# Kernel tuning notes

Hardware: AMD Instinct MI355X
Metric: run time of the kernel (lower is better)

## Reference

```python
import jax, jax.numpy as jnp
import numpy as np

B, D, T, V = 16, 128, 4096, 1024


def setup_inputs() -> dict:
    key = jax.random.key(0)
    k1, k2 = jax.random.split(key)
    latents = jax.random.normal(k1, (B, D, T), dtype=jnp.float32)
    codebook = jax.random.normal(k2, (V, D), dtype=jnp.float32)  # code_embed.weight
    return {"latents": latents, "codebook": codebook}


def reference(latents, codebook):
    # decode(): latents (B, D, T) -> (B, T, D); nearest code under L2 (torch.cdist + argmin)
    x = jnp.transpose(latents, (0, 2, 1))  # (B, T, D)
    x_sq = jnp.sum(x * x, axis=-1, keepdims=True)          # (B, T, 1)
    c_sq = jnp.sum(codebook * codebook, axis=-1)           # (V,)
    cross = jnp.einsum('btd,vd->btv', x, codebook)         # (B, T, V) -- the fusion target
    d2 = x_sq - 2.0 * cross + c_sq                         # (B, T, V)
    codes = jnp.argmin(d2, axis=-1)                        # (B, T) int
    # quantized latents: embed the chosen codes back to (B, D, T)
    quantized = jnp.transpose(codebook[codes], (0, 2, 1))  # (B, D, T)
    return codes.astype(jnp.int32), quantized
```

## Files before the change

kernel.cpp:

```cpp
#include <hip/hip_runtime.h>

#define B_ 16
#define D_ 128
#define T_ 4096
#define V_ 1024

typedef _Float16 half8 __attribute__((ext_vector_type(8)));
typedef float float4v __attribute__((ext_vector_type(4)));


__global__ __launch_bounds__(256) void split_csq_kernel(const float* __restrict__ cb,
                                                        char* __restrict__ Bc,
                                                        float* __restrict__ chsq) {
    const int g = blockIdx.x * 256 + threadIdx.x;
    const int v = g >> 4;
    const int k0 = (g & 15) << 3;
    const float* src = cb + (size_t)v * D_ + k0;
    half8 h, l;
    float s = 0.f;
#pragma unroll
    for (int j = 0; j < 8; ++j) {
        float c = src[j];
        _Float16 ch = (_Float16)c;
        h[j] = ch;
        l[j] = (_Float16)((c - (float)ch) * 2048.0f);
        s = fmaf(c, c, s);
    }
    const int kt = k0 >> 5;
    const int q = (k0 >> 3) & 3;
    const int c = v >> 5;
    const int ntl = (v >> 4) & 1;
    const int ln = v & 15;
    const size_t off =
        (size_t)c * 16384 + kt * 2048 + ntl * 1024 + (size_t)(q * 16 + ln) * 16;
    *(half8*)(Bc + off) = h;
    *(half8*)(Bc + off + 8192) = l;
#pragma unroll
    for (int o = 1; o < 16; o <<= 1) s += __shfl_xor(s, o, 64);
    if ((g & 15) == 0) chsq[v] = 0.5f * s;
}

__device__ __forceinline__ void dma16(const char* g, char* lds) {
    __builtin_amdgcn_global_load_lds(
        (const __attribute__((address_space(1))) unsigned int*)g,
        (__attribute__((address_space(3))) unsigned int*)lds, 16, 0, 0);
}

__device__ __forceinline__ void dma_chunk(char* ldsbuf, const char* Bc, int c, int wq,
                                          int tl) {
#pragma unroll
    for (int j = 0; j < 4; ++j) {
        const int seg = wq * 4 + j;
        dma16(Bc + (size_t)c * 16384 + seg * 1024 + tl * 16, ldsbuf + seg * 1024);
    }
}

__global__ __launch_bounds__(256, 2) void vq_mfma(const float* __restrict__ latents,
                                                  const float* __restrict__ codebook,
                                                  const float* __restrict__ chsq,
                                                  const char* __restrict__ Bc,
                                                  float* __restrict__ out_codes,
                                                  float* __restrict__ out_q) {
    __shared__ __align__(16) char smem[69632];
    __shared__ float sChsq[V_];
    __shared__ int scode[128];

    const int tid = threadIdx.x;
    const int tl = tid & 63;
    const int wq = tid >> 6;
    const int ln = tid & 15;
    const int q = (tid >> 4) & 3;
    const int b = blockIdx.x >> 5;
    const int t00 = (blockIdx.x & 31) << 7;

    _Float16* AhS = (_Float16*)smem;
    _Float16* AlS = AhS + 128 * 136;

#pragma unroll
    for (int i = 0; i < V_ / 256; ++i) sChsq[tid + i * 256] = chsq[tid + i * 256];

#pragma unroll
    for (int th = 0; th < 2; ++th) {
        const int row = th * 64 + tl;
        const float* xp = latents + (size_t)b * D_ * T_ + t00 + row;
#pragma unroll
        for (int i = 0; i < 4; ++i) {
            const int d0 = wq * 32 + i * 8;
            float x[8];
#pragma unroll
            for (int j = 0; j < 8; ++j) x[j] = xp[(size_t)(d0 + j) * T_];
            half8 h, l;
#pragma unroll
            for (int j = 0; j < 8; ++j) {
                _Float16 xh = (_Float16)x[j];
                h[j] = xh;
                l[j] = (_Float16)((x[j] - (float)xh) * 2048.0f);
            }
            *(half8*)(AhS + row * 136 + d0) = h;
            *(half8*)(AlS + row * 136 + d0) = l;
        }
    }
    __syncthreads();

    half8 ah[4][2], al[4][2];
#pragma unroll
    for (int kt = 0; kt < 4; ++kt)
#pragma unroll
        for (int mt = 0; mt < 2; ++mt) {
            const int row = wq * 32 + mt * 16 + ln;
            ah[kt][mt] = *(const half8*)(AhS + row * 136 + kt * 32 + q * 8);
            al[kt][mt] = *(const half8*)(AlS + row * 136 + kt * 32 + q * 8);
        }
    __syncthreads();

    char* Bb = smem;

    float bestF[2][4];
    int bestv[2][4];
#pragma unroll
    for (int mt = 0; mt < 2; ++mt)
#pragma unroll
        for (int r = 0; r < 4; ++r) {
            bestF[mt][r] = 3.0e38f;
            bestv[mt][r] = 0;
        }

    float4v acc1[2][2][2], acc2[2][2][2];

    auto fold = [&](int s, int cc) {
#pragma unroll
        for (int ntl = 0; ntl < 2; ++ntl) {
            const int n = cc * 32 + ntl * 16 + ln;
            const float csq = sChsq[n];
#pragma unroll
            for (int mt = 0; mt < 2; ++mt)
#pragma unroll
                for (int r = 0; r < 4; ++r) {
                    const float score = csq - (acc1[s][mt][ntl][r] +
                                               acc2[s][mt][ntl][r] * (1.0f / 2048.0f));
                    if (score < bestF[mt][r]) {
                        bestF[mt][r] = score;
                        bestv[mt][r] = n;
                    }
                }
        }
    };

    dma_chunk(Bb, Bc, 0, wq, tl);
    __syncthreads();

    for (int c = 0; c < 32; ++c) {
        const int set = c & 1;
        if (c + 1 < 32) dma_chunk(Bb + ((c + 1) & 1) * 16384, Bc, c + 1, wq, tl);

        const char* buf = Bb + set * 16384;
#pragma unroll
        for (int mt = 0; mt < 2; ++mt)
#pragma unroll
            for (int ntl = 0; ntl < 2; ++ntl) {
                acc1[set][mt][ntl] = (float4v){0.f, 0.f, 0.f, 0.f};
                acc2[set][mt][ntl] = (float4v){0.f, 0.f, 0.f, 0.f};
            }
#pragma unroll
        for (int kt = 0; kt < 4; ++kt) {
            half8 bh[2], bl[2];
#pragma unroll
            for (int ntl = 0; ntl < 2; ++ntl) {
                const int o = kt * 2048 + ntl * 1024 + tl * 16;
                bh[ntl] = *(const half8*)(buf + o);
                bl[ntl] = *(const half8*)(buf + 8192 + o);
            }
#pragma unroll
            for (int ntl = 0; ntl < 2; ++ntl)
#pragma unroll
                for (int mt = 0; mt < 2; ++mt) {
                    acc1[set][mt][ntl] = __builtin_amdgcn_mfma_f32_16x16x32_f16(
                        ah[kt][mt], bh[ntl], acc1[set][mt][ntl], 0, 0, 0);
                    acc2[set][mt][ntl] = __builtin_amdgcn_mfma_f32_16x16x32_f16(
                        ah[kt][mt], bl[ntl], acc2[set][mt][ntl], 0, 0, 0);
                    acc2[set][mt][ntl] = __builtin_amdgcn_mfma_f32_16x16x32_f16(
                        al[kt][mt], bh[ntl], acc2[set][mt][ntl], 0, 0, 0);
                }
        }
        if (c > 0) fold(set ^ 1, c - 1);
        __syncthreads();
    }
    fold(1, 31);

#pragma unroll
    for (int off = 1; off < 16; off <<= 1) {
#pragma unroll
        for (int mt = 0; mt < 2; ++mt)
#pragma unroll
            for (int r = 0; r < 4; ++r) {
                const float of = __shfl_xor(bestF[mt][r], off, 64);
                const int ov = __shfl_xor(bestv[mt][r], off, 64);
                if (of < bestF[mt][r] || (of == bestF[mt][r] && ov < bestv[mt][r])) {
                    bestF[mt][r] = of;
                    bestv[mt][r] = ov;
                }
            }
    }

    if (ln == 0) {
#pragma unroll
        for (int mt = 0; mt < 2; ++mt)
#pragma unroll
            for (int r = 0; r < 4; ++r) {
                const int m = wq * 32 + mt * 16 + q * 4 + r;
                scode[m] = bestv[mt][r];
                out_codes[(size_t)b * T_ + t00 + m] = (float)bestv[mt][r];
            }
    }
    __syncthreads();

#pragma unroll
    for (int th = 0; th < 2; ++th) {
        const int row = th * 64 + tl;
        const int code = scode[row];
        const float* crow = codebook + (size_t)code * D_;
        float* qp = out_q + (size_t)b * D_ * T_ + t00 + row;
#pragma unroll
        for (int i = 0; i < 32; ++i) {
            const int d = wq * 32 + i;
            qp[(size_t)d * T_] = crow[d];
        }
    }
}

extern "C" void kernel_launch(void* const* d_in, const int* in_sizes, int n_in,
                              void* d_out, int out_size, void* d_ws, size_t ws_size,
                              hipStream_t stream) {
    const float* latents = (const float*)d_in[0];
    const float* codebook = (const float*)d_in[1];

    float* out_codes = (float*)d_out;
    float* out_q = (float*)d_out + B_ * T_;

    float* chsq = (float*)d_ws;
    char* Bc = (char*)d_ws + 4096;

    split_csq_kernel<<<(V_ * 16) / 256, 256, 0, stream>>>(codebook, Bc, chsq);
    vq_mfma<<<(B_ * T_) / 128, 256, 0, stream>>>(latents, codebook, chsq, Bc, out_codes,
                                                 out_q);
}
```

Measured before the change: 138.9 us.

## Use two waves per block with 64 rows each and drop deferred fold

The main VQ kernel now runs with 128 threads (two waves) per 128-row block instead of four waves. Each wave handles 64 rows (four M tiles), so every codebook fragment read from LDS feeds twice as many MFMAs. Each thread issues twice as many DMA loads, latent loads and output stores. The deferred, double-buffered fold of accumulators is replaced by an immediate fold after each chunk, which saves registers but exposes MFMA result latency and halves the waves available to hide latency.

```diff
diff --git a/kernel.cpp b/kernel.cpp
--- a/kernel.cpp
+++ b/kernel.cpp
@@ -49,13 +49,13 @@
 __device__ __forceinline__ void dma_chunk(char* ldsbuf, const char* Bc, int c, int wq,
                                           int tl) {
 #pragma unroll
-    for (int j = 0; j < 4; ++j) {
-        const int seg = wq * 4 + j;
+    for (int j = 0; j < 8; ++j) {
+        const int seg = wq * 8 + j;
         dma16(Bc + (size_t)c * 16384 + seg * 1024 + tl * 16, ldsbuf + seg * 1024);
     }
 }
 
-__global__ __launch_bounds__(256, 2) void vq_mfma(const float* __restrict__ latents,
+__global__ __launch_bounds__(128, 1) void vq_mfma(const float* __restrict__ latents,
                                                   const float* __restrict__ codebook,
                                                   const float* __restrict__ chsq,
                                                   const char* __restrict__ Bc,
@@ -77,15 +77,15 @@
     _Float16* AlS = AhS + 128 * 136;
 
 #pragma unroll
-    for (int i = 0; i < V_ / 256; ++i) sChsq[tid + i * 256] = chsq[tid + i * 256];
+    for (int i = 0; i < V_ / 128; ++i) sChsq[tid + i * 128] = chsq[tid + i * 128];
 
 #pragma unroll
     for (int th = 0; th < 2; ++th) {
         const int row = th * 64 + tl;
         const float* xp = latents + (size_t)b * D_ * T_ + t00 + row;
 #pragma unroll
-        for (int i = 0; i < 4; ++i) {
-            const int d0 = wq * 32 + i * 8;
+        for (int i = 0; i < 8; ++i) {
+            const int d0 = wq * 64 + i * 8;
             float x[8];
 #pragma unroll
             for (int j = 0; j < 8; ++j) x[j] = xp[(size_t)(d0 + j) * T_];
@@ -102,12 +102,12 @@
     }
     __syncthreads();
 
-    half8 ah[4][2], al[4][2];
+    half8 ah[4][4], al[4][4];
 #pragma unroll
     for (int kt = 0; kt < 4; ++kt)
 #pragma unroll
-        for (int mt = 0; mt < 2; ++mt) {
-            const int row = wq * 32 + mt * 16 + ln;
+        for (int mt = 0; mt < 4; ++mt) {
+            const int row = wq * 64 + mt * 16 + ln;
             ah[kt][mt] = *(const half8*)(AhS + row * 136 + kt * 32 + q * 8);
             al[kt][mt] = *(const half8*)(AlS + row * 136 + kt * 32 + q * 8);
         }
@@ -115,82 +115,75 @@
 
     char* Bb = smem;
 
-    float bestF[2][4];
-    int bestv[2][4];
-#pragma unroll
-    for (int mt = 0; mt < 2; ++mt)
+    float bestF[4][4];
+    int bestv[4][4];
+#pragma unroll
+    for (int mt = 0; mt < 4; ++mt)
 #pragma unroll
         for (int r = 0; r < 4; ++r) {
             bestF[mt][r] = 3.0e38f;
             bestv[mt][r] = 0;
         }
 
-    float4v acc1[2][2][2], acc2[2][2][2];
-
-    auto fold = [&](int s, int cc) {
+    dma_chunk(Bb, Bc, 0, wq, tl);
+    __syncthreads();
+
+    for (int c = 0; c < 32; ++c) {
+        if (c + 1 < 32) dma_chunk(Bb + ((c + 1) & 1) * 16384, Bc, c + 1, wq, tl);
+
+        const char* buf = Bb + (c & 1) * 16384;
+        float4v acc1[4][2], acc2[4][2];
+#pragma unroll
+        for (int mt = 0; mt < 4; ++mt)
+#pragma unroll
+            for (int ntl = 0; ntl < 2; ++ntl) {
+                acc1[mt][ntl] = (float4v){0.f, 0.f, 0.f, 0.f};
+                acc2[mt][ntl] = (float4v){0.f, 0.f, 0.f, 0.f};
+            }
+#pragma unroll
+        for (int kt = 0; kt < 4; ++kt) {
+            half8 bh[2], bl[2];
+#pragma unroll
+            for (int ntl = 0; ntl < 2; ++ntl) {
+                const int o = kt * 2048 + ntl * 1024 + tl * 16;
+                bh[ntl] = *(const half8*)(buf + o);
+                bl[ntl] = *(const half8*)(buf + 8192 + o);
+            }
+#pragma unroll
+            for (int ntl = 0; ntl < 2; ++ntl)
+#pragma unroll
+                for (int mt = 0; mt < 4; ++mt) {
+                    acc1[mt][ntl] = __builtin_amdgcn_mfma_f32_16x16x32_f16(
+                        ah[kt][mt], bh[ntl], acc1[mt][ntl], 0, 0, 0);
+                    acc2[mt][ntl] = __builtin_amdgcn_mfma_f32_16x16x32_f16(
+                        ah[kt][mt], bl[ntl], acc2[mt][ntl], 0, 0, 0);
+                    acc2[mt][ntl] = __builtin_amdgcn_mfma_f32_16x16x32_f16(
+                        al[kt][mt], bh[ntl], acc2[mt][ntl], 0, 0, 0);
+                }
+        }
 #pragma unroll
         for (int ntl = 0; ntl < 2; ++ntl) {
-            const int n = cc * 32 + ntl * 16 + ln;
+            const int n = c * 32 + ntl * 16 + ln;
             const float csq = sChsq[n];
 #pragma unroll
-            for (int mt = 0; mt < 2; ++mt)
+            for (int mt = 0; mt < 4; ++mt)
 #pragma unroll
                 for (int r = 0; r < 4; ++r) {
-                    const float score = csq - (acc1[s][mt][ntl][r] +
-                                               acc2[s][mt][ntl][r] * (1.0f / 2048.0f));
+                    const float score =
+                        csq - (acc1[mt][ntl][r] + acc2[mt][ntl][r] * (1.0f / 2048.0f));
                     if (score < bestF[mt][r]) {
                         bestF[mt][r] = score;
                         bestv[mt][r] = n;
                     }
                 }
         }
-    };
-
-    dma_chunk(Bb, Bc, 0, wq, tl);
-    __syncthreads();
-
-    for (int c = 0; c < 32; ++c) {
-        const int set = c & 1;
-        if (c + 1 < 32) dma_chunk(Bb + ((c + 1) & 1) * 16384, Bc, c + 1, wq, tl);
-
-        const char* buf = Bb + set * 16384;
-#pragma unroll
-        for (int mt = 0; mt < 2; ++mt)
-#pragma unroll
-            for (int ntl = 0; ntl < 2; ++ntl) {
-                acc1[set][mt][ntl] = (float4v){0.f, 0.f, 0.f, 0.f};
-                acc2[set][mt][ntl] = (float4v){0.f, 0.f, 0.f, 0.f};
-            }
-#pragma unroll
-        for (int kt = 0; kt < 4; ++kt) {
-            half8 bh[2], bl[2];
-#pragma unroll
-            for (int ntl = 0; ntl < 2; ++ntl) {
-                const int o = kt * 2048 + ntl * 1024 + tl * 16;
-                bh[ntl] = *(const half8*)(buf + o);
-                bl[ntl] = *(const half8*)(buf + 8192 + o);
-            }
-#pragma unroll
-            for (int ntl = 0; ntl < 2; ++ntl)
-#pragma unroll
-                for (int mt = 0; mt < 2; ++mt) {
-                    acc1[set][mt][ntl] = __builtin_amdgcn_mfma_f32_16x16x32_f16(
-                        ah[kt][mt], bh[ntl], acc1[set][mt][ntl], 0, 0, 0);
-                    acc2[set][mt][ntl] = __builtin_amdgcn_mfma_f32_16x16x32_f16(
-                        ah[kt][mt], bl[ntl], acc2[set][mt][ntl], 0, 0, 0);
-                    acc2[set][mt][ntl] = __builtin_amdgcn_mfma_f32_16x16x32_f16(
-                        al[kt][mt], bh[ntl], acc2[set][mt][ntl], 0, 0, 0);
-                }
-        }
-        if (c > 0) fold(set ^ 1, c - 1);
         __syncthreads();
     }
-    fold(1, 31);
 
 #pragma unroll
     for (int off = 1; off < 16; off <<= 1) {
 #pragma unroll
-        for (int mt = 0; mt < 2; ++mt)
+        for (int mt = 0; mt < 4; ++mt)
 #pragma unroll
             for (int r = 0; r < 4; ++r) {
                 const float of = __shfl_xor(bestF[mt][r], off, 64);
@@ -204,10 +197,10 @@
 
     if (ln == 0) {
 #pragma unroll
-        for (int mt = 0; mt < 2; ++mt)
+        for (int mt = 0; mt < 4; ++mt)
 #pragma unroll
             for (int r = 0; r < 4; ++r) {
-                const int m = wq * 32 + mt * 16 + q * 4 + r;
+                const int m = wq * 64 + mt * 16 + q * 4 + r;
                 scode[m] = bestv[mt][r];
                 out_codes[(size_t)b * T_ + t00 + m] = (float)bestv[mt][r];
             }
@@ -221,8 +214,8 @@
         const float* crow = codebook + (size_t)code * D_;
         float* qp = out_q + (size_t)b * D_ * T_ + t00 + row;
 #pragma unroll
-        for (int i = 0; i < 32; ++i) {
-            const int d = wq * 32 + i;
+        for (int i = 0; i < 64; ++i) {
+            const int d = wq * 64 + i;
             qp[(size_t)d * T_] = crow[d];
         }
     }
@@ -241,6 +234,6 @@
     char* Bc = (char*)d_ws + 4096;
 
     split_csq_kernel<<<(V_ * 16) / 256, 256, 0, stream>>>(codebook, Bc, chsq);
-    vq_mfma<<<(B_ * T_) / 128, 256, 0, stream>>>(latents, codebook, chsq, Bc, out_codes,
+    vq_mfma<<<(B_ * T_) / 128, 128, 0, stream>>>(latents, codebook, chsq, Bc, out_codes,
                                                  out_q);
 }
```

Result: slower. 144.6 us (+4.1%).

## Halve LDS footprint and drop deferred fold to raise occupancy to three blocks

Applied to the files above, without the earlier changes.

Staging of the split-fp16 latent tile now happens in two 64-row halves, so shared memory shrinks from about 68KB to 34KB. Launch bounds go from 2 to 3 blocks per CU. The double-buffered accumulators and the fold deferred by one chunk are removed, and each chunk is folded right after its MFMAs, which cuts register pressure. The cost is an extra barrier pair during staging, and the loss of overlap between each chunk's fold and the next chunk's MFMAs.

```diff
diff --git a/kernel.cpp b/kernel.cpp
--- a/kernel.cpp
+++ b/kernel.cpp
@@ -55,13 +55,13 @@
     }
 }
 
-__global__ __launch_bounds__(256, 2) void vq_mfma(const float* __restrict__ latents,
+__global__ __launch_bounds__(256, 3) void vq_mfma(const float* __restrict__ latents,
                                                   const float* __restrict__ codebook,
                                                   const float* __restrict__ chsq,
                                                   const char* __restrict__ Bc,
                                                   float* __restrict__ out_codes,
                                                   float* __restrict__ out_q) {
-    __shared__ __align__(16) char smem[69632];
+    __shared__ __align__(16) char smem[34816];
     __shared__ float sChsq[V_];
     __shared__ int scode[128];
 
@@ -73,16 +73,17 @@
     const int b = blockIdx.x >> 5;
     const int t00 = (blockIdx.x & 31) << 7;
 
+#pragma unroll
+    for (int i = 0; i < V_ / 256; ++i) sChsq[tid + i * 256] = chsq[tid + i * 256];
+
     _Float16* AhS = (_Float16*)smem;
-    _Float16* AlS = AhS + 128 * 136;
-
-#pragma unroll
-    for (int i = 0; i < V_ / 256; ++i) sChsq[tid + i * 256] = chsq[tid + i * 256];
-
-#pragma unroll
-    for (int th = 0; th < 2; ++th) {
-        const int row = th * 64 + tl;
-        const float* xp = latents + (size_t)b * D_ * T_ + t00 + row;
+    _Float16* AlS = AhS + 64 * 136;
+
+    half8 ah[4][2], al[4][2];
+#pragma unroll
+    for (int half = 0; half < 2; ++half) {
+        const int grow = half * 64 + tl;
+        const float* xp = latents + (size_t)b * D_ * T_ + t00 + grow;
 #pragma unroll
         for (int i = 0; i < 4; ++i) {
             const int d0 = wq * 32 + i * 8;
@@ -96,22 +97,22 @@
                 h[j] = xh;
                 l[j] = (_Float16)((x[j] - (float)xh) * 2048.0f);
             }
-            *(half8*)(AhS + row * 136 + d0) = h;
-            *(half8*)(AlS + row * 136 + d0) = l;
-        }
-    }
-    __syncthreads();
-
-    half8 ah[4][2], al[4][2];
-#pragma unroll
-    for (int kt = 0; kt < 4; ++kt)
-#pragma unroll
-        for (int mt = 0; mt < 2; ++mt) {
-            const int row = wq * 32 + mt * 16 + ln;
-            ah[kt][mt] = *(const half8*)(AhS + row * 136 + kt * 32 + q * 8);
-            al[kt][mt] = *(const half8*)(AlS + row * 136 + kt * 32 + q * 8);
-        }
-    __syncthreads();
+            *(half8*)(AhS + tl * 136 + d0) = h;
+            *(half8*)(AlS + tl * 136 + d0) = l;
+        }
+        __syncthreads();
+        if ((wq >> 1) == half) {
+#pragma unroll
+            for (int kt = 0; kt < 4; ++kt)
+#pragma unroll
+                for (int mt = 0; mt < 2; ++mt) {
+                    const int r2 = (wq & 1) * 32 + mt * 16 + ln;
+                    ah[kt][mt] = *(const half8*)(AhS + r2 * 136 + kt * 32 + q * 8);
+                    al[kt][mt] = *(const half8*)(AlS + r2 * 136 + kt * 32 + q * 8);
+                }
+        }
+        __syncthreads();
+    }
 
     char* Bb = smem;
 
@@ -125,67 +126,60 @@
             bestv[mt][r] = 0;
         }
 
-    float4v acc1[2][2][2], acc2[2][2][2];
-
-    auto fold = [&](int s, int cc) {
+    dma_chunk(Bb, Bc, 0, wq, tl);
+    __syncthreads();
+
+    for (int c = 0; c < 32; ++c) {
+        if (c + 1 < 32) dma_chunk(Bb + ((c + 1) & 1) * 16384, Bc, c + 1, wq, tl);
+
+        const char* buf = Bb + (c & 1) * 16384;
+        float4v acc1[2][2], acc2[2][2];
+#pragma unroll
+        for (int mt = 0; mt < 2; ++mt)
+#pragma unroll
+            for (int ntl = 0; ntl < 2; ++ntl) {
+                acc1[mt][ntl] = (float4v){0.f, 0.f, 0.f, 0.f};
+                acc2[mt][ntl] = (float4v){0.f, 0.f, 0.f, 0.f};
+            }
+#pragma unroll
+        for (int kt = 0; kt < 4; ++kt) {
+            half8 bh[2], bl[2];
+#pragma unroll
+            for (int ntl = 0; ntl < 2; ++ntl) {
+                const int o = kt * 2048 + ntl * 1024 + tl * 16;
+                bh[ntl] = *(const half8*)(buf + o);
+                bl[ntl] = *(const half8*)(buf + 8192 + o);
+            }
+#pragma unroll
+            for (int ntl = 0; ntl < 2; ++ntl)
+#pragma unroll
+                for (int mt = 0; mt < 2; ++mt) {
+                    acc1[mt][ntl] = __builtin_amdgcn_mfma_f32_16x16x32_f16(
+                        ah[kt][mt], bh[ntl], acc1[mt][ntl], 0, 0, 0);
+                    acc2[mt][ntl] = __builtin_amdgcn_mfma_f32_16x16x32_f16(
+                        ah[kt][mt], bl[ntl], acc2[mt][ntl], 0, 0, 0);
+                    acc2[mt][ntl] = __builtin_amdgcn_mfma_f32_16x16x32_f16(
+                        al[kt][mt], bh[ntl], acc2[mt][ntl], 0, 0, 0);
+                }
+        }
 #pragma unroll
         for (int ntl = 0; ntl < 2; ++ntl) {
-            const int n = cc * 32 + ntl * 16 + ln;
+            const int n = c * 32 + ntl * 16 + ln;
             const float csq = sChsq[n];
 #pragma unroll
             for (int mt = 0; mt < 2; ++mt)
 #pragma unroll
                 for (int r = 0; r < 4; ++r) {
-                    const float score = csq - (acc1[s][mt][ntl][r] +
-                                               acc2[s][mt][ntl][r] * (1.0f / 2048.0f));
+                    const float score =
+                        csq - (acc1[mt][ntl][r] + acc2[mt][ntl][r] * (1.0f / 2048.0f));
                     if (score < bestF[mt][r]) {
                         bestF[mt][r] = score;
                         bestv[mt][r] = n;
                     }
                 }
         }
-    };
-
-    dma_chunk(Bb, Bc, 0, wq, tl);
-    __syncthreads();
-
-    for (int c = 0; c < 32; ++c) {
-        const int set = c & 1;
-        if (c + 1 < 32) dma_chunk(Bb + ((c + 1) & 1) * 16384, Bc, c + 1, wq, tl);
-
-        const char* buf = Bb + set * 16384;
-#pragma unroll
-        for (int mt = 0; mt < 2; ++mt)
-#pragma unroll
-            for (int ntl = 0; ntl < 2; ++ntl) {
-                acc1[set][mt][ntl] = (float4v){0.f, 0.f, 0.f, 0.f};
-                acc2[set][mt][ntl] = (float4v){0.f, 0.f, 0.f, 0.f};
-            }
-#pragma unroll
-        for (int kt = 0; kt < 4; ++kt) {
-            half8 bh[2], bl[2];
-#pragma unroll
-            for (int ntl = 0; ntl < 2; ++ntl) {
-                const int o = kt * 2048 + ntl * 1024 + tl * 16;
-                bh[ntl] = *(const half8*)(buf + o);
-                bl[ntl] = *(const half8*)(buf + 8192 + o);
-            }
-#pragma unroll
-            for (int ntl = 0; ntl < 2; ++ntl)
-#pragma unroll
-                for (int mt = 0; mt < 2; ++mt) {
-                    acc1[set][mt][ntl] = __builtin_amdgcn_mfma_f32_16x16x32_f16(
-                        ah[kt][mt], bh[ntl], acc1[set][mt][ntl], 0, 0, 0);
-                    acc2[set][mt][ntl] = __builtin_amdgcn_mfma_f32_16x16x32_f16(
-                        ah[kt][mt], bl[ntl], acc2[set][mt][ntl], 0, 0, 0);
-                    acc2[set][mt][ntl] = __builtin_amdgcn_mfma_f32_16x16x32_f16(
-                        al[kt][mt], bh[ntl], acc2[set][mt][ntl], 0, 0, 0);
-                }
-        }
-        if (c > 0) fold(set ^ 1, c - 1);
         __syncthreads();
     }
-    fold(1, 31);
 
 #pragma unroll
     for (int off = 1; off < 16; off <<= 1) {
```

Result: faster. 130.9 us (-5.8%).
